# Optimization experiments

Hardware: AMD Instinct MI355X
Metric: run time of the kernel (lower is better)

## Reference

```python
import jax, jax.numpy as jnp
import numpy as np

B, N, DIM, OUT_C, K_ORDERS = 4096, 17, 512, 3, 3  # K=2 -> 3 Chebyshev orders
EPS = 1e-6


def setup_inputs() -> dict:
    key = jax.random.key(0)
    ks = jax.random.split(key, 7)
    x = jax.random.normal(ks[0], (B, N, DIM), dtype=jnp.float32)
    a = jax.random.uniform(ks[1], (N, N), dtype=jnp.float32)
    adj = 0.5 * (a + a.T)  # symmetric, positive row sums
    c = jax.random.normal(ks[2], (B, 1, DIM), dtype=jnp.float32)
    # adaLN modulation: Linear(dim -> 2*dim)
    W_mod = jax.random.normal(ks[3], (DIM, 2 * DIM), dtype=jnp.float32) * (1.0 / np.sqrt(DIM))
    b_mod = jnp.zeros((2 * DIM,), dtype=jnp.float32)
    # ChebConv weights: [K+1, in_c, out_c] (squeezed broadcast dim), bias [out_c]
    Wg = jax.random.normal(ks[4], (K_ORDERS, DIM, OUT_C), dtype=jnp.float32) * (1.0 / np.sqrt(DIM))
    bg = jnp.zeros((OUT_C,), dtype=jnp.float32)
    return {"x": x, "adj": adj, "c": c, "W_mod": W_mod, "b_mod": b_mod, "Wg": Wg, "bg": bg}


def reference(x, adj, c, W_mod, b_mod, Wg, bg):
    # adaLN modulation: SiLU -> Linear -> chunk into shift/scale along dim=2
    h = jax.nn.silu(c) @ W_mod + b_mod                      # [B, 1, 2*DIM]
    shift, scale = jnp.split(h, 2, axis=2)                  # each [B, 1, DIM]
    # LayerNorm (no affine, eps=1e-6) + modulate
    mu = jnp.mean(x, axis=-1, keepdims=True)
    var = jnp.var(x, axis=-1, keepdims=True)
    xn = (x - mu) * jax.lax.rsqrt(var + EPS)
    xm = xn * (1.0 + scale) + shift                         # [B, N, DIM]
    # Normalized Laplacian: L = I - D^{-1/2} A D^{-1/2}
    d = jax.lax.rsqrt(jnp.sum(adj, axis=-1))                # [N]
    L = jnp.eye(adj.shape[0], dtype=adj.dtype) - d[:, None] * adj * d[None, :]
    # Chebyshev polynomials applied to features: T0=x, T1=Lx, T2=(2L^2 - I)x
    T0 = xm
    T1 = jnp.einsum('nm,bmc->bnc', L, xm)
    T2 = 2.0 * jnp.einsum('nm,bmc->bnc', L, T1) - T0
    # Per-order projections, summed over orders, plus bias
    out = (jnp.einsum('bnc,co->bno', T0, Wg[0])
           + jnp.einsum('bnc,co->bno', T1, Wg[1])
           + jnp.einsum('bnc,co->bno', T2, Wg[2])) + bg     # [B, N, 3]
    return out
```

## Files before the change

kernel.cpp:

```cpp
#include <hip/hip_runtime.h>
#include <hip/hip_bf16.h>
#include <stdint.h>

typedef __attribute__((ext_vector_type(8))) short short8;
typedef __attribute__((ext_vector_type(4))) float f32x4;

#define NBATCH 4096
#define NNODE  17
#define NDIM   512
#define ROWLEN 8704

__device__ __forceinline__ unsigned short f2bf(float f) {
    union { float f; unsigned int u; } v; v.f = f;
    unsigned int r = v.u + 0x7fffu + ((v.u >> 16) & 1u);
    return (unsigned short)(r >> 16);
}
__device__ __forceinline__ unsigned int pk2(unsigned short a, unsigned short b) {
    return (unsigned int)a | ((unsigned int)b << 16);
}
__device__ __forceinline__ float silu_f(float x) {
    return x / (1.0f + __expf(-x));
}

__global__ __launch_bounds__(256) void prep_kernel(
        const float* __restrict__ cin, const float* __restrict__ Wmod,
        unsigned short* __restrict__ cb, unsigned short* __restrict__ wbT) {
    int bid = blockIdx.x;
    int tid = threadIdx.x;
    if (bid < 128) {
        __shared__ float tile[64][65];
        int txt = bid & 15, tyt = bid >> 4;
        int cx = tid & 63, ry = tid >> 6;
        #pragma unroll
        for (int rr = 0; rr < 16; ++rr) {
            int r = ry + rr * 4;
            tile[r][cx] = Wmod[(tyt*64 + r) * 1024 + txt*64 + cx];
        }
        __syncthreads();
        #pragma unroll
        for (int rr = 0; rr < 16; ++rr) {
            int r = ry + rr * 4;
            wbT[(txt*64 + r) * 512 + tyt*64 + cx] = f2bf(tile[cx][r]);
        }
    } else {
        int t = (bid - 128) * 256 + tid;
        const float4* s = reinterpret_cast<const float4*>(cin) + (size_t)t * 2;
        float4 a = s[0], b = s[1];
        uint4 o;
        o.x = pk2(f2bf(silu_f(a.x)), f2bf(silu_f(a.y)));
        o.y = pk2(f2bf(silu_f(a.z)), f2bf(silu_f(a.w)));
        o.z = pk2(f2bf(silu_f(b.x)), f2bf(silu_f(b.y)));
        o.w = pk2(f2bf(silu_f(b.z)), f2bf(silu_f(b.w)));
        *reinterpret_cast<uint4*>(cb + (size_t)t * 8) = o;
    }
}

__global__ __launch_bounds__(256) void gemm_kernel(
        const unsigned short* __restrict__ cb, const unsigned short* __restrict__ wbT,
        const float* __restrict__ b_mod, float* __restrict__ H) {
    int w = threadIdx.x >> 6, l = threadIdx.x & 63;
    int lr = l & 15, lk = (l >> 4) * 8;
    int rowbase = blockIdx.y * 128 + w * 32;
    int colbase = blockIdx.x * 64;
    f32x4 acc[2][4] = {};
    for (int kk = 0; kk < 16; ++kk) {
        int k = kk * 32 + lk;
        short8 a0 = *reinterpret_cast<const short8*>(cb + (size_t)(rowbase + lr) * 512 + k);
        short8 a1 = *reinterpret_cast<const short8*>(cb + (size_t)(rowbase + 16 + lr) * 512 + k);
        #pragma unroll
        for (int j = 0; j < 4; ++j) {
            short8 bv = *reinterpret_cast<const short8*>(wbT + (size_t)(colbase + j*16 + lr) * 512 + k);
            acc[0][j] = __builtin_amdgcn_mfma_f32_16x16x32_bf16(a0, bv, acc[0][j], 0, 0, 0);
            acc[1][j] = __builtin_amdgcn_mfma_f32_16x16x32_bf16(a1, bv, acc[1][j], 0, 0, 0);
        }
    }
    #pragma unroll
    for (int j = 0; j < 4; ++j) {
        int col = colbase + j * 16 + lr;
        float bm = b_mod[col];
        #pragma unroll
        for (int i = 0; i < 2; ++i) {
            int row0 = rowbase + i * 16 + (l >> 4) * 4;
            #pragma unroll
            for (int r = 0; r < 4; ++r)
                H[(size_t)(row0 + r) * 1024 + col] = acc[i][j][r] + bm;
        }
    }
}

__global__ __launch_bounds__(512) void main_kernel(
        const float* __restrict__ x, const float* __restrict__ adj,
        const float* __restrict__ Wg, const float* __restrict__ bg,
        const float* __restrict__ H, float* __restrict__ out) {
    __shared__ __align__(16) unsigned short xm_lds[32][520];
    __shared__ __align__(16) unsigned short wg_lds[16][520];
    __shared__ float L_lds[17][18];
    __shared__ float P_lds[32][16];
    __shared__ float Q_lds[17][4];
    __shared__ float S_lds[12];

    int b = blockIdx.x;
    int tid = threadIdx.x;
    int w = tid >> 6, l = tid & 63;

    if (w == 7) {
        for (int c = l; c < 512; c += 64) {
            float f = 1.0f + H[(size_t)b * 1024 + 512 + c];
            #pragma unroll
            for (int k = 0; k < 3; ++k)
                #pragma unroll
                for (int o = 0; o < 3; ++o)
                    wg_lds[k*3 + o][c] = f2bf(f * Wg[k*1536 + c*3 + o]);
        }
    } else if (w == 6) {
        float dv = 0.0f;
        if (l < 17) {
            float rs = 0.0f;
            #pragma unroll
            for (int j = 0; j < 17; ++j) rs += adj[l*17 + j];
            dv = rsqrtf(rs);
        }
        for (int e = l; e < 289; e += 64) {
            int i = e / 17, j = e - i * 17;
            float di = __shfl(dv, i), dj = __shfl(dv, j);
            L_lds[i][j] = (i == j ? 1.0f : 0.0f) - di * adj[e] * dj;
        }
    } else if (w == 2) {
        float p0=0,p1=0,p2=0,p3=0,p4=0,p5=0,p6=0,p7=0,p8=0;
        for (int c = l; c < 512; c += 64) {
            float shv = H[(size_t)b * 1024 + c];
            const float* wr = Wg + c * 3;
            p0 += shv * wr[0];      p1 += shv * wr[1];      p2 += shv * wr[2];
            p3 += shv * wr[1536];   p4 += shv * wr[1537];   p5 += shv * wr[1538];
            p6 += shv * wr[3072];   p7 += shv * wr[3073];   p8 += shv * wr[3074];
        }
        #pragma unroll
        for (int m = 1; m < 64; m <<= 1) {
            p0 += __shfl_xor(p0, m); p1 += __shfl_xor(p1, m); p2 += __shfl_xor(p2, m);
            p3 += __shfl_xor(p3, m); p4 += __shfl_xor(p4, m); p5 += __shfl_xor(p5, m);
            p6 += __shfl_xor(p6, m); p7 += __shfl_xor(p7, m); p8 += __shfl_xor(p8, m);
        }
        if (l == 0) {
            S_lds[0]=p0; S_lds[1]=p1; S_lds[2]=p2; S_lds[3]=p3; S_lds[4]=p4;
            S_lds[5]=p5; S_lds[6]=p6; S_lds[7]=p7; S_lds[8]=p8;
        }
    }

    const float* xb = x + (size_t)b * ROWLEN;
    for (int n = w; n < 17; n += 8) {
        const float4* xp = reinterpret_cast<const float4*>(xb + n * 512 + 8 * l);
        float4 v0 = xp[0], v1 = xp[1];
        float xv[8] = {v0.x, v0.y, v0.z, v0.w, v1.x, v1.y, v1.z, v1.w};
        float s = 0.0f, s2 = 0.0f;
        #pragma unroll
        for (int j = 0; j < 8; ++j) { s += xv[j]; s2 += xv[j] * xv[j]; }
        #pragma unroll
        for (int m = 1; m < 64; m <<= 1) { s += __shfl_xor(s, m); s2 += __shfl_xor(s2, m); }
        float mu = s * (1.0f / 512.0f);
        float var = s2 * (1.0f / 512.0f) - mu * mu;
        float rstd = rsqrtf(var + 1e-6f);
        unsigned short hv[8];
        #pragma unroll
        for (int j = 0; j < 8; ++j) hv[j] = f2bf((xv[j] - mu) * rstd);
        uint4 ov;
        ov.x = pk2(hv[0], hv[1]); ov.y = pk2(hv[2], hv[3]);
        ov.z = pk2(hv[4], hv[5]); ov.w = pk2(hv[6], hv[7]);
        *reinterpret_cast<uint4*>(&xm_lds[n][8 * l]) = ov;
    }
    __syncthreads();

    if (w < 2) {
        int lr = l & 15, lk = (l >> 4) * 8;
        f32x4 acc = {0.f, 0.f, 0.f, 0.f};
        #pragma unroll
        for (int kk = 0; kk < 16; ++kk) {
            int k = kk * 32 + lk;
            short8 av = *reinterpret_cast<const short8*>(&xm_lds[w * 16 + lr][k]);
            short8 bv = *reinterpret_cast<const short8*>(&wg_lds[lr][k]);
            acc = __builtin_amdgcn_mfma_f32_16x16x32_bf16(av, bv, acc, 0, 0, 0);
        }
        int pr = w * 16 + (l >> 4) * 4;
        #pragma unroll
        for (int r = 0; r < 4; ++r) P_lds[pr + r][lr] = acc[r];
    }
    __syncthreads();

    if (tid < 153) {
        int n = tid / 9, r = tid - n * 9;
        P_lds[n][r] += S_lds[r];
    }
    __syncthreads();

    if (tid < 51) {
        int n = tid / 3, o = tid - n * 3;
        float q = 0.0f;
        #pragma unroll
        for (int m = 0; m < 17; ++m) q += L_lds[n][m] * P_lds[m][6 + o];
        Q_lds[n][o] = q;
    }
    __syncthreads();

    if (tid < 51) {
        int n = tid / 3, o = tid - n * 3;
        float r = P_lds[n][o] - P_lds[n][6 + o] + bg[o];
        #pragma unroll
        for (int m = 0; m < 17; ++m)
            r += L_lds[n][m] * (P_lds[m][3 + o] + 2.0f * Q_lds[m][o]);
        out[(size_t)b * 51 + tid] = r;
    }
}

extern "C" void kernel_launch(void* const* d_in, const int* in_sizes, int n_in,
                              void* d_out, int out_size, void* d_ws, size_t ws_size,
                              hipStream_t stream) {
    const float* x     = (const float*)d_in[0];
    const float* adj   = (const float*)d_in[1];
    const float* c     = (const float*)d_in[2];
    const float* W_mod = (const float*)d_in[3];
    const float* b_mod = (const float*)d_in[4];
    const float* Wg    = (const float*)d_in[5];
    const float* bg    = (const float*)d_in[6];
    float* out = (float*)d_out;

    unsigned short* cb  = (unsigned short*)d_ws;
    unsigned short* wbT = (unsigned short*)((char*)d_ws + (4u << 20));
    float*          H   = (float*)((char*)d_ws + (5u << 20));

    prep_kernel<<<1152, 256, 0, stream>>>(c, W_mod, cb, wbT);
    gemm_kernel<<<dim3(16, 32), 256, 0, stream>>>(cb, wbT, b_mod, H);
    main_kernel<<<4096, 512, 0, stream>>>(x, adj, Wg, bg, H, out);
}
```

Baseline: 263.0 us.

## Process two batches per block with fp32 projections and precomputed Laplacian

The main kernel now handles two batch items per 512-thread block. Each wave loads all of its node rows into registers up front, and the projection onto the 9 weight columns is done in fp32 by dot product and wave reduction instead of bf16 MFMA. The normalized Laplacian is computed once in the prep kernel rather than in every block, and the shift term is treated as an extra pseudo-node. The intent is to cut per-block setup and improve memory-level parallelism; the cost is more register pressure from the launch bound and longer shuffle reductions.

```diff
diff --git a/kernel.cpp b/kernel.cpp
--- a/kernel.cpp
+++ b/kernel.cpp
@@ -24,12 +24,28 @@
 
 __global__ __launch_bounds__(256) void prep_kernel(
         const float* __restrict__ cin, const float* __restrict__ Wmod,
-        unsigned short* __restrict__ cb, unsigned short* __restrict__ wbT) {
+        const float* __restrict__ adj,
+        unsigned short* __restrict__ cb, unsigned short* __restrict__ wbT,
+        float* __restrict__ Lw) {
     int bid = blockIdx.x;
     int tid = threadIdx.x;
-    if (bid < 128) {
+    if (bid == 0) {
+        __shared__ float dsh[17];
+        if (tid < 17) {
+            float rs = 0.0f;
+            #pragma unroll
+            for (int j = 0; j < 17; ++j) rs += adj[tid * 17 + j];
+            dsh[tid] = rsqrtf(rs);
+        }
+        __syncthreads();
+        for (int e = tid; e < 289; e += 256) {
+            int i = e / 17, j = e - i * 17;
+            Lw[e] = (i == j ? 1.0f : 0.0f) - dsh[i] * adj[e] * dsh[j];
+        }
+    } else if (bid < 129) {
         __shared__ float tile[64][65];
-        int txt = bid & 15, tyt = bid >> 4;
+        int bt = bid - 1;
+        int txt = bt & 15, tyt = bt >> 4;
         int cx = tid & 63, ry = tid >> 6;
         #pragma unroll
         for (int rr = 0; rr < 16; ++rr) {
@@ -43,7 +59,7 @@
             wbT[(txt*64 + r) * 512 + tyt*64 + cx] = f2bf(tile[cx][r]);
         }
     } else {
-        int t = (bid - 128) * 256 + tid;
+        int t = (bid - 129) * 256 + tid;
         const float4* s = reinterpret_cast<const float4*>(cin) + (size_t)t * 2;
         float4 a = s[0], b = s[1];
         uint4 o;
@@ -88,125 +104,130 @@
     }
 }
 
-__global__ __launch_bounds__(512) void main_kernel(
-        const float* __restrict__ x, const float* __restrict__ adj,
+__global__ __launch_bounds__(512, 4) void main_kernel(
+        const float* __restrict__ x, const float* __restrict__ Lw,
         const float* __restrict__ Wg, const float* __restrict__ bg,
         const float* __restrict__ H, float* __restrict__ out) {
-    __shared__ __align__(16) unsigned short xm_lds[32][520];
-    __shared__ __align__(16) unsigned short wg_lds[16][520];
-    __shared__ float L_lds[17][18];
-    __shared__ float P_lds[32][16];
-    __shared__ float Q_lds[17][4];
-    __shared__ float S_lds[12];
-
-    int b = blockIdx.x;
+    __shared__ float Wt[9][520];
+    __shared__ float L_s[17][20];
+    __shared__ float P_s[2][18][12];
+
     int tid = threadIdx.x;
     int w = tid >> 6, l = tid & 63;
-
-    if (w == 7) {
-        for (int c = l; c < 512; c += 64) {
-            float f = 1.0f + H[(size_t)b * 1024 + 512 + c];
-            #pragma unroll
-            for (int k = 0; k < 3; ++k)
-                #pragma unroll
-                for (int o = 0; o < 3; ++o)
-                    wg_lds[k*3 + o][c] = f2bf(f * Wg[k*1536 + c*3 + o]);
-        }
-    } else if (w == 6) {
-        float dv = 0.0f;
-        if (l < 17) {
-            float rs = 0.0f;
-            #pragma unroll
-            for (int j = 0; j < 17; ++j) rs += adj[l*17 + j];
-            dv = rsqrtf(rs);
-        }
-        for (int e = l; e < 289; e += 64) {
-            int i = e / 17, j = e - i * 17;
-            float di = __shfl(dv, i), dj = __shfl(dv, j);
-            L_lds[i][j] = (i == j ? 1.0f : 0.0f) - di * adj[e] * dj;
-        }
-    } else if (w == 2) {
-        float p0=0,p1=0,p2=0,p3=0,p4=0,p5=0,p6=0,p7=0,p8=0;
-        for (int c = l; c < 512; c += 64) {
-            float shv = H[(size_t)b * 1024 + c];
-            const float* wr = Wg + c * 3;
-            p0 += shv * wr[0];      p1 += shv * wr[1];      p2 += shv * wr[2];
-            p3 += shv * wr[1536];   p4 += shv * wr[1537];   p5 += shv * wr[1538];
-            p6 += shv * wr[3072];   p7 += shv * wr[3073];   p8 += shv * wr[3074];
-        }
-        #pragma unroll
-        for (int m = 1; m < 64; m <<= 1) {
-            p0 += __shfl_xor(p0, m); p1 += __shfl_xor(p1, m); p2 += __shfl_xor(p2, m);
-            p3 += __shfl_xor(p3, m); p4 += __shfl_xor(p4, m); p5 += __shfl_xor(p5, m);
-            p6 += __shfl_xor(p6, m); p7 += __shfl_xor(p7, m); p8 += __shfl_xor(p8, m);
-        }
-        if (l == 0) {
-            S_lds[0]=p0; S_lds[1]=p1; S_lds[2]=p2; S_lds[3]=p3; S_lds[4]=p4;
-            S_lds[5]=p5; S_lds[6]=p6; S_lds[7]=p7; S_lds[8]=p8;
-        }
-    }
-
-    const float* xb = x + (size_t)b * ROWLEN;
-    for (int n = w; n < 17; n += 8) {
-        const float4* xp = reinterpret_cast<const float4*>(xb + n * 512 + 8 * l);
-        float4 v0 = xp[0], v1 = xp[1];
-        float xv[8] = {v0.x, v0.y, v0.z, v0.w, v1.x, v1.y, v1.z, v1.w};
-        float s = 0.0f, s2 = 0.0f;
-        #pragma unroll
-        for (int j = 0; j < 8; ++j) { s += xv[j]; s2 += xv[j] * xv[j]; }
-        #pragma unroll
-        for (int m = 1; m < 64; m <<= 1) { s += __shfl_xor(s, m); s2 += __shfl_xor(s2, m); }
-        float mu = s * (1.0f / 512.0f);
-        float var = s2 * (1.0f / 512.0f) - mu * mu;
-        float rstd = rsqrtf(var + 1e-6f);
-        unsigned short hv[8];
-        #pragma unroll
-        for (int j = 0; j < 8; ++j) hv[j] = f2bf((xv[j] - mu) * rstd);
-        uint4 ov;
-        ov.x = pk2(hv[0], hv[1]); ov.y = pk2(hv[2], hv[3]);
-        ov.z = pk2(hv[4], hv[5]); ov.w = pk2(hv[6], hv[7]);
-        *reinterpret_cast<uint4*>(&xm_lds[n][8 * l]) = ov;
+    int b0 = blockIdx.x * 2;
+
+    float xv[5][8];
+    int tslot[5], tnode[5];
+    #pragma unroll
+    for (int i = 0; i < 5; ++i) {
+        int t = w + i * 8;
+        int tc = t < 36 ? t : 35;
+        int slot = tc >= 18 ? 1 : 0;
+        int node = tc - slot * 18;
+        tslot[i] = slot; tnode[i] = node;
+        const float* src = (node < 17)
+            ? x + (size_t)(b0 + slot) * ROWLEN + node * 512 + 8 * l
+            : H + (size_t)(b0 + slot) * 1024 + 8 * l;
+        float4 a = reinterpret_cast<const float4*>(src)[0];
+        float4 c4 = reinterpret_cast<const float4*>(src)[1];
+        xv[i][0]=a.x;  xv[i][1]=a.y;  xv[i][2]=a.z;  xv[i][3]=a.w;
+        xv[i][4]=c4.x; xv[i][5]=c4.y; xv[i][6]=c4.z; xv[i][7]=c4.w;
+    }
+    float fs0[8], fs1[8];
+    {
+        const float4* h0 = reinterpret_cast<const float4*>(H + (size_t)b0 * 1024 + 512 + 8 * l);
+        const float4* h1 = reinterpret_cast<const float4*>(H + (size_t)(b0 + 1) * 1024 + 512 + 8 * l);
+        float4 a = h0[0], b = h0[1], c4 = h1[0], d4 = h1[1];
+        fs0[0]=1.f+a.x; fs0[1]=1.f+a.y; fs0[2]=1.f+a.z; fs0[3]=1.f+a.w;
+        fs0[4]=1.f+b.x; fs0[5]=1.f+b.y; fs0[6]=1.f+b.z; fs0[7]=1.f+b.w;
+        fs1[0]=1.f+c4.x; fs1[1]=1.f+c4.y; fs1[2]=1.f+c4.z; fs1[3]=1.f+c4.w;
+        fs1[4]=1.f+d4.x; fs1[5]=1.f+d4.y; fs1[6]=1.f+d4.z; fs1[7]=1.f+d4.w;
+    }
+
+    {
+        int c = tid;
+        #pragma unroll
+        for (int k = 0; k < 3; ++k) {
+            float w0 = Wg[k * 1536 + c * 3 + 0];
+            float w1 = Wg[k * 1536 + c * 3 + 1];
+            float w2 = Wg[k * 1536 + c * 3 + 2];
+            Wt[k * 3 + 0][c] = w0;
+            Wt[k * 3 + 1][c] = w1;
+            Wt[k * 3 + 2][c] = w2;
+        }
+    }
+    if (tid < 289) {
+        int i2 = tid / 17, j2 = tid - i2 * 17;
+        L_s[i2][j2] = Lw[tid];
     }
     __syncthreads();
 
-    if (w < 2) {
-        int lr = l & 15, lk = (l >> 4) * 8;
-        f32x4 acc = {0.f, 0.f, 0.f, 0.f};
-        #pragma unroll
-        for (int kk = 0; kk < 16; ++kk) {
-            int k = kk * 32 + lk;
-            short8 av = *reinterpret_cast<const short8*>(&xm_lds[w * 16 + lr][k]);
-            short8 bv = *reinterpret_cast<const short8*>(&wg_lds[lr][k]);
-            acc = __builtin_amdgcn_mfma_f32_16x16x32_bf16(av, bv, acc, 0, 0, 0);
-        }
-        int pr = w * 16 + (l >> 4) * 4;
-        #pragma unroll
-        for (int r = 0; r < 4; ++r) P_lds[pr + r][lr] = acc[r];
+    #pragma unroll
+    for (int i = 0; i < 5; ++i) {
+        int t = w + i * 8;
+        if (t < 36) {
+            float xs[8];
+            if (tnode[i] < 17) {
+                float s = 0.0f, s2 = 0.0f;
+                #pragma unroll
+                for (int j = 0; j < 8; ++j) { s += xv[i][j]; s2 += xv[i][j] * xv[i][j]; }
+                #pragma unroll
+                for (int m = 1; m < 64; m <<= 1) { s += __shfl_xor(s, m); s2 += __shfl_xor(s2, m); }
+                float mu = s * (1.0f / 512.0f);
+                float var = s2 * (1.0f / 512.0f) - mu * mu;
+                float rstd = rsqrtf(var + 1e-6f);
+                #pragma unroll
+                for (int j = 0; j < 8; ++j) {
+                    float fj = tslot[i] ? fs1[j] : fs0[j];
+                    xs[j] = (xv[i][j] - mu) * rstd * fj;
+                }
+            } else {
+                #pragma unroll
+                for (int j = 0; j < 8; ++j) xs[j] = xv[i][j];
+            }
+            float p[9];
+            #pragma unroll
+            for (int r = 0; r < 9; ++r) {
+                float4 w0 = *reinterpret_cast<const float4*>(&Wt[r][8 * l]);
+                float4 w1 = *reinterpret_cast<const float4*>(&Wt[r][8 * l + 4]);
+                p[r] = xs[0]*w0.x + xs[1]*w0.y + xs[2]*w0.z + xs[3]*w0.w
+                     + xs[4]*w1.x + xs[5]*w1.y + xs[6]*w1.z + xs[7]*w1.w;
+            }
+            #pragma unroll
+            for (int m = 1; m < 64; m <<= 1) {
+                #pragma unroll
+                for (int r = 0; r < 9; ++r) p[r] += __shfl_xor(p[r], m);
+            }
+            if (l == 0) {
+                #pragma unroll
+                for (int r = 0; r < 9; ++r) P_s[tslot[i]][tnode[i]][r] = p[r];
+            }
+        }
     }
     __syncthreads();
 
-    if (tid < 153) {
-        int n = tid / 9, r = tid - n * 9;
-        P_lds[n][r] += S_lds[r];
+    if (tid < 102) {
+        int slot = tid / 51, q = tid - slot * 51;
+        int n = q / 3, o = q - n * 3;
+        float s2v = P_s[slot][17][6 + o];
+        float acc = 0.0f;
+        #pragma unroll
+        for (int m = 0; m < 17; ++m) acc += L_s[n][m] * (P_s[slot][m][6 + o] + s2v);
+        P_s[slot][n][9 + o] = acc;
     }
     __syncthreads();
 
-    if (tid < 51) {
-        int n = tid / 3, o = tid - n * 3;
-        float q = 0.0f;
-        #pragma unroll
-        for (int m = 0; m < 17; ++m) q += L_lds[n][m] * P_lds[m][6 + o];
-        Q_lds[n][o] = q;
-    }
-    __syncthreads();
-
-    if (tid < 51) {
-        int n = tid / 3, o = tid - n * 3;
-        float r = P_lds[n][o] - P_lds[n][6 + o] + bg[o];
+    if (tid < 102) {
+        int slot = tid / 51, q = tid - slot * 51;
+        int n = q / 3, o = q - n * 3;
+        float s0v = P_s[slot][17][o];
+        float s1v = P_s[slot][17][3 + o];
+        float s2v = P_s[slot][17][6 + o];
+        float r = P_s[slot][n][o] + s0v - P_s[slot][n][6 + o] - s2v + bg[o];
         #pragma unroll
         for (int m = 0; m < 17; ++m)
-            r += L_lds[n][m] * (P_lds[m][3 + o] + 2.0f * Q_lds[m][o]);
-        out[(size_t)b * 51 + tid] = r;
+            r += L_s[n][m] * (P_s[slot][m][3 + o] + s1v + 2.0f * P_s[slot][m][9 + o]);
+        out[(size_t)(b0 + slot) * 51 + q] = r;
     }
 }
 
@@ -225,8 +246,9 @@
     unsigned short* cb  = (unsigned short*)d_ws;
     unsigned short* wbT = (unsigned short*)((char*)d_ws + (4u << 20));
     float*          H   = (float*)((char*)d_ws + (5u << 20));
-
-    prep_kernel<<<1152, 256, 0, stream>>>(c, W_mod, cb, wbT);
+    float*          Lw  = (float*)((char*)d_ws + (21u << 20));
+
+    prep_kernel<<<1153, 256, 0, stream>>>(c, W_mod, adj, cb, wbT, Lw);
     gemm_kernel<<<dim3(16, 32), 256, 0, stream>>>(cb, wbT, b_mod, H);
-    main_kernel<<<4096, 512, 0, stream>>>(x, adj, Wg, bg, H, out);
-}
+    main_kernel<<<2048, 512, 0, stream>>>(x, Lw, Wg, bg, H, out);
+}
```

After: 294.5 us. +12.0%, slower.
